# Optimization experiments

Hardware: AMD Instinct MI355X
Metric: run time of the kernel (lower is better)

The kernel has to match this reference:

```python
import jax, jax.numpy as jnp
import numpy as np

SCALE = 500.0  # config.scale
RADIUS = 1.1   # config.radius


def setup_inputs() -> dict:
    key = jax.random.key(0)
    k1, k2, k3 = jax.random.split(key, 3)
    N, D, T, R, B = 65536, 3, 64, 64, 64
    x = jax.random.normal(k1, (N, D), dtype=jnp.float32)
    directions = jax.random.normal(k2, (D, T), dtype=jnp.float32)
    directions = directions / jnp.linalg.norm(directions, axis=0, keepdims=True)  # unit directions
    lin = jnp.linspace(-RADIUS, RADIUS, R, dtype=jnp.float32)
    batch = jnp.sort(jax.random.randint(k3, (N,), 0, B)).astype(jnp.int64)
    return {"x": x, "directions": directions, "lin": lin, "batch": batch, "dim_size": B}


def reference(x, directions, lin, batch, dim_size):
    # nh: height of each point along each direction. [N, T]
    nh = x @ directions
    N, T = nh.shape
    R = lin.shape[0]
    # Sigmoid-smoothed indicator of (height <= threshold). [N, R, T]
    ecc = jax.nn.sigmoid(SCALE * (lin[None, :, None] - nh[:, None, :]))
    # Scatter-accumulate per point cloud. [B, R, T]
    ect = jax.ops.segment_sum(
        ecc.reshape(N, R * T), batch, num_segments=dim_size,
        indices_are_sorted=True,
    ).reshape(dim_size, R, T)
    return ect
```

## Files before the change

kernel.cpp:

```cpp
#include <hip/hip_runtime.h>


#define T_DIRS   64
#define R_STEPS  64
#define NROWS    65
#define N_BATCH  64
#define TSPLIT   16
#define TQW      4
#define PSW      16
#define THREADS  512
#define NWAVES   8
#define SSTRIDE  256
#define MAXSAMP  512

#define RADIUS_F 1.1f
#define STEP_F   (2.0f * RADIUS_F / (R_STEPS - 1))
#define INV_STEP (1.0f / STEP_F)
#define OFF_F    (RADIUS_F * INV_STEP)
#define MEXP     (-500.0f * STEP_F * 1.4426950408889634f)
#define FIXP     512.0f
#define INV_FIXP (1.0f / 512.0f)
#define CNT_ONE  (1u << 20)
#define SI_MASK  0xFFFFFu

__global__ __launch_bounds__(THREADS) void ect_kernel(
    const float* __restrict__ x,
    const float* __restrict__ dirs,
    const int*   __restrict__ batch,
    float* __restrict__ out,
    int N)
{
    __shared__ unsigned s_a[NROWS * TQW];
    __shared__ unsigned s_ws[NWAVES * TQW];
    __shared__ int      s_samp[MAXSAMP];
    __shared__ int      s_ks_lo, s_ks_hi, s_lo, s_hi;

    const int tid  = threadIdx.x;
    const int b    = blockIdx.x >> 4;
    const int q    = blockIdx.x & (TSPLIT - 1);
    const int lane = tid & 63;
    const int w    = tid >> 6;
    const int ps   = lane >> 2;
    const int tq   = lane & (TQW - 1);
    const int tg   = q * TQW + tq;

    const int nsamp = (N + SSTRIDE - 1) / SSTRIDE;

    for (int i = tid; i < NROWS * TQW; i += THREADS) s_a[i] = 0u;
    if (tid == 0) { s_ks_lo = nsamp; s_ks_hi = nsamp; s_lo = N; s_hi = N; }
    for (int k = tid; k < nsamp; k += THREADS) s_samp[k] = batch[k * SSTRIDE];

    const float d0 = dirs[tg];
    const float d1 = dirs[T_DIRS + tg];
    const float d2 = dirs[2 * T_DIRS + tg];
    __syncthreads();

    for (int k = tid; k < nsamp; k += THREADS) {
        int v  = s_samp[k];
        int vp = (k == 0) ? -1 : s_samp[k - 1];
        if (v >= b && vp < b)  s_ks_lo = k;
        if (v >  b && vp <= b) s_ks_hi = k;
    }
    __syncthreads();

    if (tid <= SSTRIDE) {
        int kl = s_ks_lo, kh = s_ks_hi;
        int w0 = (kl == 0) ? 0 : (kl - 1) * SSTRIDE;
        int w1 = (kl >= nsamp) ? N : min(N, kl * SSTRIDE + 1);
        int j  = w0 + tid;
        if (j < w1) {
            int v  = batch[j];
            int vp = (j == 0) ? -1 : batch[j - 1];
            if (v >= b && vp < b) s_lo = j;
        }
        int h0 = (kh == 0) ? 0 : (kh - 1) * SSTRIDE;
        int h1 = (kh >= nsamp) ? N : min(N, kh * SSTRIDE + 1);
        j = h0 + tid;
        if (j < h1) {
            int v  = batch[j];
            int vp = (j == 0) ? -1 : batch[j - 1];
            if (v > b && vp <= b) s_hi = j;
        }
    }
    __syncthreads();
    const int lo = s_lo, hi = s_hi;
    const int len = hi - lo;
    const float* xb = x + (size_t)lo * 3;

    for (int p = w * PSW + ps; p < len; p += NWAVES * PSW) {
        float x0 = xb[p * 3 + 0];
        float x1 = xb[p * 3 + 1];
        float x2 = xb[p * 3 + 2];
        float nh  = fmaf(x2, d2, fmaf(x1, d1, x0 * d0));
        float u   = fmaf(nh, INV_STEP, OFF_F);
        float r0f = rintf(u);
        float dd  = r0f - u;
        float e   = __builtin_amdgcn_exp2f(dd * MEXP);
        float s   = __builtin_amdgcn_rcpf(1.0f + e);
        unsigned si = (unsigned)fmaf(s, FIXP, 0.5f);
        int j1 = (int)r0f + 1;
        if (j1 <= R_STEPS) {
            j1 = max(j1, 0);
            atomicAdd(&s_a[j1 * TQW + tq], CNT_ONE | si);
        }
    }
    __syncthreads();

    const int rl = ps & 7;
    unsigned c = s_a[(8 * w + rl) * TQW + tq] >> 20;
    unsigned wsum = c;
    wsum += __shfl_xor(wsum, 4, 64);
    wsum += __shfl_xor(wsum, 8, 64);
    wsum += __shfl_xor(wsum, 16, 64);
    if (lane < TQW) s_ws[w * TQW + tq] = wsum;
    __syncthreads();

    if (ps < 8) {
        unsigned run = 0;
        for (int w2 = 0; w2 < w; ++w2) run += s_ws[w2 * TQW + tq];
#pragma unroll
        for (int i = 0; i < 8; ++i)
            if (i <= rl) run += s_a[(8 * w + i) * TQW + tq] >> 20;
        unsigned si = s_a[(8 * w + rl + 1) * TQW + tq] & SI_MASK;
        int r = 8 * w + rl;
        out[((size_t)b << 12) | (r << 6) | tg] =
            (float)run + (float)si * INV_FIXP;
    }
}

extern "C" void kernel_launch(void* const* d_in, const int* in_sizes, int n_in,
                              void* d_out, int out_size, void* d_ws, size_t ws_size,
                              hipStream_t stream) {
    const float* x     = (const float*)d_in[0];
    const float* dirs  = (const float*)d_in[1];
    const int*   batch = (const int*)d_in[3];
    float* out = (float*)d_out;
    const int N = in_sizes[3];

    ect_kernel<<<dim3(N_BATCH * TSPLIT), dim3(THREADS), 0, stream>>>(
        x, dirs, batch, out, N);
}
```

Before: 12.62 us.

## Find segment bounds with windowed scan near expected offsets; single-wave scan epilogue

Replaces the two-level sampled search for each batch segment's start and end with a direct scan of a fixed window around the position expected for uniformly sized segments, falling back to a full scan when the boundary is not found. This removes the sample load pass, one barrier and the coarse-search shared array. The epilogue now has a single wave read the 65 histogram rows as uint4, compute the prefix sum with shuffles and write float4 outputs, dropping the cross-wave partial-sum pass and one barrier. The window assumes roughly equal segment sizes; skewed inputs take the slow full-scan path.

```diff
diff --git a/kernel.cpp b/kernel.cpp
--- a/kernel.cpp
+++ b/kernel.cpp
@@ -10,8 +10,7 @@
 #define PSW      16
 #define THREADS  512
 #define NWAVES   8
-#define SSTRIDE  256
-#define MAXSAMP  512
+#define WIN      768
 
 #define RADIUS_F 1.1f
 #define STEP_F   (2.0f * RADIUS_F / (R_STEPS - 1))
@@ -31,9 +30,7 @@
     int N)
 {
     __shared__ unsigned s_a[NROWS * TQW];
-    __shared__ unsigned s_ws[NWAVES * TQW];
-    __shared__ int      s_samp[MAXSAMP];
-    __shared__ int      s_ks_lo, s_ks_hi, s_lo, s_hi;
+    __shared__ int      s_lo, s_hi;
 
     const int tid  = threadIdx.x;
     const int b    = blockIdx.x >> 4;
@@ -44,46 +41,44 @@
     const int tq   = lane & (TQW - 1);
     const int tg   = q * TQW + tq;
 
-    const int nsamp = (N + SSTRIDE - 1) / SSTRIDE;
-
     for (int i = tid; i < NROWS * TQW; i += THREADS) s_a[i] = 0u;
-    if (tid == 0) { s_ks_lo = nsamp; s_ks_hi = nsamp; s_lo = N; s_hi = N; }
-    for (int k = tid; k < nsamp; k += THREADS) s_samp[k] = batch[k * SSTRIDE];
+    if (tid == 0) { s_lo = -1; s_hi = -1; }
 
     const float d0 = dirs[tg];
     const float d1 = dirs[T_DIRS + tg];
     const float d2 = dirs[2 * T_DIRS + tg];
     __syncthreads();
 
-    for (int k = tid; k < nsamp; k += THREADS) {
-        int v  = s_samp[k];
-        int vp = (k == 0) ? -1 : s_samp[k - 1];
-        if (v >= b && vp < b)  s_ks_lo = k;
-        if (v >  b && vp <= b) s_ks_hi = k;
-    }
-    __syncthreads();
-
-    if (tid <= SSTRIDE) {
-        int kl = s_ks_lo, kh = s_ks_hi;
-        int w0 = (kl == 0) ? 0 : (kl - 1) * SSTRIDE;
-        int w1 = (kl >= nsamp) ? N : min(N, kl * SSTRIDE + 1);
-        int j  = w0 + tid;
-        if (j < w1) {
+    {
+        const int seg = N >> 6;
+        int c0 = b * seg;
+        int a0 = max(0, c0 - WIN), a1 = min(N, c0 + WIN);
+        for (int j = a0 + tid; j < a1; j += THREADS) {
             int v  = batch[j];
             int vp = (j == 0) ? -1 : batch[j - 1];
             if (v >= b && vp < b) s_lo = j;
         }
-        int h0 = (kh == 0) ? 0 : (kh - 1) * SSTRIDE;
-        int h1 = (kh >= nsamp) ? N : min(N, kh * SSTRIDE + 1);
-        j = h0 + tid;
-        if (j < h1) {
+        int c1 = (b + 1) * seg;
+        int b0 = max(0, c1 - WIN), b1 = min(N, c1 + WIN);
+        for (int j = b0 + tid; j < b1; j += THREADS) {
             int v  = batch[j];
             int vp = (j == 0) ? -1 : batch[j - 1];
             if (v > b && vp <= b) s_hi = j;
         }
     }
     __syncthreads();
-    const int lo = s_lo, hi = s_hi;
+
+    if (s_lo < 0 || s_hi < 0) {
+        for (int j = tid; j < N; j += THREADS) {
+            int v  = batch[j];
+            int vp = (j == 0) ? -1 : batch[j - 1];
+            if (v >= b && vp < b)  s_lo = j;
+            if (v >  b && vp <= b) s_hi = j;
+        }
+        __syncthreads();
+    }
+    const int lo  = (s_lo < 0) ? N : s_lo;
+    const int hi  = (s_hi < 0) ? N : s_hi;
     const int len = hi - lo;
     const float* xb = x + (size_t)lo * 3;
 
@@ -105,27 +100,36 @@
         }
     }
     __syncthreads();
+    if (w != 0) return;
 
-    const int rl = ps & 7;
-    unsigned c = s_a[(8 * w + rl) * TQW + tq] >> 20;
-    unsigned wsum = c;
-    wsum += __shfl_xor(wsum, 4, 64);
-    wsum += __shfl_xor(wsum, 8, 64);
-    wsum += __shfl_xor(wsum, 16, 64);
-    if (lane < TQW) s_ws[w * TQW + tq] = wsum;
-    __syncthreads();
+    uint4 rowv = *(const uint4*)&s_a[lane * TQW];
+    uint4 r64  = *(const uint4*)&s_a[R_STEPS * TQW];
 
-    if (ps < 8) {
-        unsigned run = 0;
-        for (int w2 = 0; w2 < w; ++w2) run += s_ws[w2 * TQW + tq];
+    unsigned c0 = rowv.x >> 20, c1 = rowv.y >> 20,
+             c2 = rowv.z >> 20, c3 = rowv.w >> 20;
+    unsigned s0 = rowv.x & SI_MASK, s1 = rowv.y & SI_MASK,
+             s2 = rowv.z & SI_MASK, s3 = rowv.w & SI_MASK;
+
+    unsigned n0 = __shfl_down(s0, 1, 64), n1 = __shfl_down(s1, 1, 64),
+             n2 = __shfl_down(s2, 1, 64), n3 = __shfl_down(s3, 1, 64);
+    if (lane == 63) {
+        n0 = r64.x & SI_MASK; n1 = r64.y & SI_MASK;
+        n2 = r64.z & SI_MASK; n3 = r64.w & SI_MASK;
+    }
+
 #pragma unroll
-        for (int i = 0; i < 8; ++i)
-            if (i <= rl) run += s_a[(8 * w + i) * TQW + tq] >> 20;
-        unsigned si = s_a[(8 * w + rl + 1) * TQW + tq] & SI_MASK;
-        int r = 8 * w + rl;
-        out[((size_t)b << 12) | (r << 6) | tg] =
-            (float)run + (float)si * INV_FIXP;
+    for (int d = 1; d < 64; d <<= 1) {
+        unsigned u0 = __shfl_up(c0, d, 64), u1 = __shfl_up(c1, d, 64),
+                 u2 = __shfl_up(c2, d, 64), u3 = __shfl_up(c3, d, 64);
+        if (lane >= d) { c0 += u0; c1 += u1; c2 += u2; c3 += u3; }
     }
+
+    float4 o;
+    o.x = (float)c0 + (float)n0 * INV_FIXP;
+    o.y = (float)c1 + (float)n1 * INV_FIXP;
+    o.z = (float)c2 + (float)n2 * INV_FIXP;
+    o.w = (float)c3 + (float)n3 * INV_FIXP;
+    *(float4*)&out[((size_t)b << 12) | (lane << 6) | (q * TQW)] = o;
 }
 
 extern "C" void kernel_launch(void* const* d_in, const int* in_sizes, int n_in,
```

Result: slower. 34.22 us (+171.2%).
